# Performance work log

Hardware: AMD Instinct MI355X
Metric: run time of the kernel (lower is better)

The kernel has to match this reference:

```python
import jax, jax.numpy as jnp
import numpy as np

NUM_HEADS = 12


def setup_inputs() -> dict:
    key = jax.random.key(0)
    k1, k2, k3 = jax.random.split(key, 3)
    B, S, E = 1, 4096, 768
    x = jax.random.normal(k1, (B, S, E), dtype=jnp.float32)
    # learned parameters (nn.Linear weights, stored as [in, out] for x @ W)
    w_qkv = jax.random.normal(k2, (E, 3 * E), dtype=jnp.float32) * 0.02
    b_qkv = jnp.zeros((3 * E,), dtype=jnp.float32)
    w_out = jax.random.normal(k3, (E, E), dtype=jnp.float32) * 0.02
    b_out = jnp.zeros((E,), dtype=jnp.float32)
    return {"x": x, "w_qkv": w_qkv, "b_qkv": b_qkv, "w_out": w_out, "b_out": b_out}


def reference(x, w_qkv, b_qkv, w_out, b_out):
    """Single-process (world_size==1) path of the module:
    qkv projection -> multi-head scaled-dot-product softmax attention
    (non-causal) -> output projection. Dropout is identity in eval.
    """
    B, S, E = x.shape
    H = NUM_HEADS
    D = E // H
    scale = 1.0 / jnp.sqrt(jnp.asarray(D, dtype=x.dtype))

    qkv = x @ w_qkv + b_qkv                       # [B, S, 3E]
    qkv = qkv.reshape(B, S, 3, H, D)
    qkv = jnp.transpose(qkv, (2, 0, 3, 1, 4))     # [3, B, H, S, D]
    q, k, v = qkv[0], qkv[1], qkv[2]

    scores = jnp.einsum("bhqd,bhkd->bhqk", q * scale, k)  # [B, H, S, S]
    attn = jax.nn.softmax(scores, axis=-1)
    out = jnp.einsum("bhqk,bhkd->bhqd", attn, v)           # [B, H, S, D]

    out = jnp.transpose(out, (0, 2, 1, 3)).reshape(B, S, E)
    return out @ w_out + b_out
```

## Files before the change

### kernel.cpp

```cpp
#include <hip/hip_runtime.h>

typedef __attribute__((ext_vector_type(8))) short bh8;
typedef __attribute__((ext_vector_type(4))) float fx4;

__device__ __forceinline__ unsigned short f2bf(float f) {
    unsigned int u = __float_as_uint(f);
    u += 0x7FFF + ((u >> 16) & 1);
    return (unsigned short)(u >> 16);
}

__device__ __forceinline__ unsigned int cvtpk_bf16(float a, float b) {
    unsigned int r;
    asm("v_cvt_pk_bf16_f32 %0, %1, %2" : "=v"(r) : "v"(a), "v"(b));
    return r;
}

__device__ __forceinline__ bh8 pack4(unsigned int a, unsigned int b,
                                     unsigned int c, unsigned int d) {
    union { unsigned int u[4]; bh8 h; } z;
    z.u[0] = a; z.u[1] = b; z.u[2] = c; z.u[3] = d;
    return z.h;
}

__device__ __forceinline__ void stage_rows8(const unsigned short* g, long ldg,
                                            unsigned short* lds, int lane) {
    int r8 = lane >> 3;
    int gc = (lane & 7) ^ r8;
    __builtin_amdgcn_global_load_lds(
        (const __attribute__((address_space(1))) void*)(g + (long)r8 * ldg + gc * 8),
        (__attribute__((address_space(3))) void*)lds, 16, 0, 0);
}

__device__ __forceinline__ bh8 frag_ld(const unsigned short* t, int row, int kchunk, int lane) {
    int ch = (kchunk + (lane >> 4)) ^ (row & 7);
    return *(const bh8*)(t + row * 64 + ch * 8);
}

__global__ __launch_bounds__(256) void castbf(const float* __restrict__ x,
                                              unsigned short* __restrict__ y, int n) {
    int i = (blockIdx.x * 256 + threadIdx.x) * 4;
    if (i < n) {
        float4 v = *(const float4*)(x + i);
        ushort4 o = make_ushort4(f2bf(v.x), f2bf(v.y), f2bf(v.z), f2bf(v.w));
        *(ushort4*)(y + i) = o;
    }
}

__global__ __launch_bounds__(256) void transW(const float* __restrict__ W,
                                              unsigned short* __restrict__ Wt,
                                              int K, int N) {
    __shared__ float t[32][33];
    const int n0 = blockIdx.x * 32, k0 = blockIdx.y * 32;
    const int tx = threadIdx.x & 31, ty = threadIdx.x >> 5;
    #pragma unroll
    for (int r = ty; r < 32; r += 8)
        t[r][tx] = W[(size_t)(k0 + r) * N + n0 + tx];
    __syncthreads();
    #pragma unroll
    for (int r = ty; r < 32; r += 8)
        Wt[(size_t)(n0 + r) * K + k0 + tx] = f2bf(t[tx][r]);
}

__global__ __launch_bounds__(256) void transV(const unsigned short* __restrict__ qkv,
                                              unsigned short* __restrict__ vt) {
    __shared__ unsigned short t[64][65];
    const int s0 = blockIdx.x * 64, h = blockIdx.y;
    const int tx = threadIdx.x & 63, ty = threadIdx.x >> 6;
    #pragma unroll
    for (int r = ty; r < 64; r += 4)
        t[r][tx] = qkv[(size_t)(s0 + r) * 2304 + 1536 + h * 64 + tx];
    __syncthreads();
    const int px = (tx & 32) + ((tx & 16) >> 2) + ((tx & 12) << 1) + (tx & 3);
    #pragma unroll
    for (int r = ty; r < 64; r += 4)
        vt[((size_t)h * 64 + r) * 4096 + s0 + px] = t[tx][r];
}

__global__ __launch_bounds__(256) void gemm_qkv(const unsigned short* __restrict__ A,
                                                const unsigned short* __restrict__ Bt,
                                                const float* __restrict__ bias,
                                                unsigned short* __restrict__ Cout,
                                                int M, int N, int K) {
    __shared__ __align__(16) unsigned short Ash[64 * 64];
    __shared__ __align__(16) unsigned short Bsh[128 * 64];
    const int m0 = blockIdx.y * 64, n0 = blockIdx.x * 128;
    const int tid = threadIdx.x, wid = tid >> 6, lane = tid & 63;
    const int wr = (wid >> 1) * 32, wc = (wid & 1) * 64;

    fx4 acc[2][4];
    #pragma unroll
    for (int i = 0; i < 2; ++i)
        #pragma unroll
        for (int j = 0; j < 4; ++j)
            acc[i][j] = (fx4){0.f, 0.f, 0.f, 0.f};

    for (int k0 = 0; k0 < K; k0 += 64) {
        #pragma unroll
        for (int g = 0; g < 2; ++g) {
            int rt = (wid * 2 + g) * 8;
            stage_rows8(A + (size_t)(m0 + rt) * K + k0, K, Ash + rt * 64, lane);
        }
        #pragma unroll
        for (int g = 0; g < 4; ++g) {
            int rt = (wid * 4 + g) * 8;
            stage_rows8(Bt + (size_t)(n0 + rt) * K + k0, K, Bsh + rt * 64, lane);
        }
        __syncthreads();
        #pragma unroll
        for (int ks = 0; ks < 2; ++ks) {
            bh8 af[2], bfr[4];
            #pragma unroll
            for (int i = 0; i < 2; ++i) af[i] = frag_ld(Ash, wr + i * 16 + (lane & 15), ks * 4, lane);
            #pragma unroll
            for (int j = 0; j < 4; ++j) bfr[j] = frag_ld(Bsh, wc + j * 16 + (lane & 15), ks * 4, lane);
            #pragma unroll
            for (int i = 0; i < 2; ++i)
                #pragma unroll
                for (int j = 0; j < 4; ++j)
                    acc[i][j] = __builtin_amdgcn_mfma_f32_16x16x32_bf16(af[i], bfr[j], acc[i][j], 0, 0, 0);
        }
        __syncthreads();
    }

    const int cc = lane & 15, g4 = (lane >> 4) * 4;
    #pragma unroll
    for (int j = 0; j < 4; ++j) {
        int col = n0 + wc + j * 16 + cc;
        float bv = bias[col];
        float sc = (col < 768) ? 0.18033688011112042f : 1.0f;
        #pragma unroll
        for (int i = 0; i < 2; ++i) {
            #pragma unroll
            for (int r = 0; r < 4; ++r) {
                int row = m0 + wr + i * 16 + g4 + r;
                Cout[(size_t)row * N + col] = f2bf((acc[i][j][r] + bv) * sc);
            }
        }
    }
}

__global__ __launch_bounds__(256) void gemm64(const unsigned short* __restrict__ A,
                                              const unsigned short* __restrict__ Bt,
                                              const float* __restrict__ bias,
                                              float* __restrict__ Cout,
                                              int M, int N, int K) {
    __shared__ __align__(16) unsigned short Ash[64 * 64];
    __shared__ __align__(16) unsigned short Bsh[64 * 64];
    const int m0 = blockIdx.y * 64, n0 = blockIdx.x * 64;
    const int tid = threadIdx.x, wid = tid >> 6, lane = tid & 63;
    const int wr = (wid >> 1) * 32, wc = (wid & 1) * 32;

    fx4 acc[2][2];
    #pragma unroll
    for (int i = 0; i < 2; ++i)
        #pragma unroll
        for (int j = 0; j < 2; ++j)
            acc[i][j] = (fx4){0.f, 0.f, 0.f, 0.f};

    for (int k0 = 0; k0 < K; k0 += 64) {
        #pragma unroll
        for (int g = 0; g < 2; ++g) {
            int rt = (wid * 2 + g) * 8;
            stage_rows8(A + (size_t)(m0 + rt) * K + k0, K, Ash + rt * 64, lane);
            stage_rows8(Bt + (size_t)(n0 + rt) * K + k0, K, Bsh + rt * 64, lane);
        }
        __syncthreads();
        #pragma unroll
        for (int ks = 0; ks < 2; ++ks) {
            bh8 af[2], bfr[2];
            #pragma unroll
            for (int i = 0; i < 2; ++i) af[i] = frag_ld(Ash, wr + i * 16 + (lane & 15), ks * 4, lane);
            #pragma unroll
            for (int j = 0; j < 2; ++j) bfr[j] = frag_ld(Bsh, wc + j * 16 + (lane & 15), ks * 4, lane);
            #pragma unroll
            for (int i = 0; i < 2; ++i)
                #pragma unroll
                for (int j = 0; j < 2; ++j)
                    acc[i][j] = __builtin_amdgcn_mfma_f32_16x16x32_bf16(af[i], bfr[j], acc[i][j], 0, 0, 0);
        }
        __syncthreads();
    }

    const int cc = lane & 15, g4 = (lane >> 4) * 4;
    #pragma unroll
    for (int j = 0; j < 2; ++j) {
        int col = n0 + wc + j * 16 + cc;
        float bv = bias[col];
        #pragma unroll
        for (int i = 0; i < 2; ++i) {
            #pragma unroll
            for (int r = 0; r < 4; ++r) {
                int row = m0 + wr + i * 16 + g4 + r;
                Cout[(size_t)row * N + col] = acc[i][j][r] + bv;
            }
        }
    }
}

__global__ __launch_bounds__(256) void attn_fwd(const unsigned short* __restrict__ qkv,
                                                const unsigned short* __restrict__ vt,
                                                unsigned short* __restrict__ ao) {
    __shared__ __align__(16) char smem[40960];
    unsigned short* Qs  = (unsigned short*)smem;
    unsigned short* Ks0 = (unsigned short*)(smem + 8192);
    unsigned short* Ks1 = (unsigned short*)(smem + 16384);
    unsigned short* Vs0 = (unsigned short*)(smem + 24576);
    unsigned short* Vs1 = (unsigned short*)(smem + 32768);
    float* Of    = (float*)smem;
    float* l_lds = (float*)(smem + 17408);

    const int h = blockIdx.y, q0 = blockIdx.x * 64;
    const int tid = threadIdx.x, wid = tid >> 6, lane = tid & 63;
    const int g = lane >> 4, qc = lane & 15, x = qc & 7;
    const int wq = wid >> 1, wk = wid & 1;

    const unsigned short* qg_ = qkv + (size_t)q0 * 2304 + h * 64;
    const unsigned short* kgb = qkv + 768 + h * 64;
    const unsigned short* vgb = vt + (size_t)h * 64 * 4096;

    #pragma unroll
    for (int gg = 0; gg < 2; ++gg) {
        int rt = (wid * 2 + gg) * 8;
        stage_rows8(qg_ + (size_t)rt * 2304, 2304, Qs + rt * 64, lane);
        stage_rows8(kgb + (size_t)rt * 2304, 2304, Ks0 + rt * 64, lane);
        stage_rows8(vgb + (size_t)rt * 4096, 4096, Vs0 + rt * 64, lane);
    }
    __syncthreads();

    bh8 qf[2][2];
    #pragma unroll
    for (int qg = 0; qg < 2; ++qg)
        #pragma unroll
        for (int kc = 0; kc < 2; ++kc)
            qf[qg][kc] = frag_ld(Qs, 32 * wq + 16 * qg + qc, 4 * kc, lane);

    int koff[2][2], voff[4];
    #pragma unroll
    for (int jm = 0; jm < 2; ++jm)
        #pragma unroll
        for (int kc = 0; kc < 2; ++kc)
            koff[jm][kc] = (32 * wk + 16 * jm + qc) * 64 + ((4 * kc + g) ^ x) * 8;
    #pragma unroll
    for (int dj = 0; dj < 4; ++dj)
        voff[dj] = (16 * dj + qc) * 64 + ((4 * wk + g) ^ x) * 8;

    float lrun[2] = {0.f, 0.f};
    fx4 oacP[4][2];
    #pragma unroll
    for (int dj = 0; dj < 4; ++dj)
        #pragma unroll
        for (int qg = 0; qg < 2; ++qg)
            oacP[dj][qg] = (fx4){0.f, 0.f, 0.f, 0.f};

    const unsigned short* knext = kgb + (size_t)64 * 2304;
    const unsigned short* vnext = vgb + 64;

    auto tile_step = [&](const unsigned short* Kc, const unsigned short* Vc,
                         unsigned short* Kd, unsigned short* Vd, bool pref) {
        if (pref) {
            #pragma unroll
            for (int gg = 0; gg < 2; ++gg) {
                int rt = (wid * 2 + gg) * 8;
                stage_rows8(knext + (size_t)rt * 2304, 2304, Kd + rt * 64, lane);
                stage_rows8(vnext + (size_t)rt * 4096, 4096, Vd + rt * 64, lane);
            }
            knext += (size_t)64 * 2304;
            vnext += 64;
        }

        bh8 kf[2][2];
        #pragma unroll
        for (int jm = 0; jm < 2; ++jm) {
            kf[jm][0] = *(const bh8*)(Kc + koff[jm][0]);
            kf[jm][1] = *(const bh8*)(Kc + koff[jm][1]);
        }
        fx4 sT[2][2];
        __builtin_amdgcn_s_setprio(1);
        #pragma unroll
        for (int jm = 0; jm < 2; ++jm)
            #pragma unroll
            for (int qg = 0; qg < 2; ++qg) {
                fx4 z = (fx4){0.f, 0.f, 0.f, 0.f};
                z = __builtin_amdgcn_mfma_f32_16x16x32_bf16(kf[jm][0], qf[qg][0], z, 0, 0, 0);
                z = __builtin_amdgcn_mfma_f32_16x16x32_bf16(kf[jm][1], qf[qg][1], z, 0, 0, 0);
                sT[jm][qg] = z;
            }
        __builtin_amdgcn_s_setprio(0);

        #pragma unroll
        for (int jm = 0; jm < 2; ++jm)
            #pragma unroll
            for (int qg = 0; qg < 2; ++qg) {
                sT[jm][qg][0] = __builtin_amdgcn_exp2f(sT[jm][qg][0]);
                sT[jm][qg][1] = __builtin_amdgcn_exp2f(sT[jm][qg][1]);
                sT[jm][qg][2] = __builtin_amdgcn_exp2f(sT[jm][qg][2]);
                sT[jm][qg][3] = __builtin_amdgcn_exp2f(sT[jm][qg][3]);
                lrun[qg] += (sT[jm][qg][0] + sT[jm][qg][1]) + (sT[jm][qg][2] + sT[jm][qg][3]);
            }

        bh8 vf[4];
        #pragma unroll
        for (int dj = 0; dj < 4; ++dj) vf[dj] = *(const bh8*)(Vc + voff[dj]);
        __builtin_amdgcn_s_setprio(1);
        #pragma unroll
        for (int qg = 0; qg < 2; ++qg) {
            bh8 pb = pack4(cvtpk_bf16(sT[0][qg][0], sT[0][qg][1]),
                           cvtpk_bf16(sT[0][qg][2], sT[0][qg][3]),
                           cvtpk_bf16(sT[1][qg][0], sT[1][qg][1]),
                           cvtpk_bf16(sT[1][qg][2], sT[1][qg][3]));
            #pragma unroll
            for (int dj = 0; dj < 4; ++dj)
                oacP[dj][qg] = __builtin_amdgcn_mfma_f32_16x16x32_bf16(vf[dj], pb, oacP[dj][qg], 0, 0, 0);
        }
        __builtin_amdgcn_s_setprio(0);
        __syncthreads();
    };

    for (int t2 = 0; t2 < 32; ++t2) {
        tile_step(Ks0, Vs0, Ks1, Vs1, true);
        tile_step(Ks1, Vs1, Ks0, Vs0, t2 < 31);
    }

    #pragma unroll
    for (int qg = 0; qg < 2; ++qg) {
        lrun[qg] += __shfl_xor(lrun[qg], 16);
        lrun[qg] += __shfl_xor(lrun[qg], 32);
    }
    if (wk == 1) {
        #pragma unroll
        for (int qg = 0; qg < 2; ++qg) {
            int q = 32 * wq + 16 * qg + qc;
            #pragma unroll
            for (int dj = 0; dj < 4; ++dj)
                *(fx4*)(Of + q * 68 + 16 * dj + 4 * g) = oacP[dj][qg];
            l_lds[q] = lrun[qg];
        }
    }
    __syncthreads();
    if (wk == 0) {
        #pragma unroll
        for (int qg = 0; qg < 2; ++qg) {
            int q = 32 * wq + 16 * qg + qc;
            float inv = 1.0f / (lrun[qg] + l_lds[q]);
            unsigned short* aop = ao + (size_t)(q0 + q) * 768 + h * 64;
            #pragma unroll
            for (int dj = 0; dj < 4; ++dj) {
                fx4 o = oacP[dj][qg];
                fx4 p = *(const fx4*)(Of + q * 68 + 16 * dj + 4 * g);
                int d0 = dj * 16 + 4 * g;
                *(unsigned int*)(aop + d0)     = cvtpk_bf16((o[0] + p[0]) * inv, (o[1] + p[1]) * inv);
                *(unsigned int*)(aop + d0 + 2) = cvtpk_bf16((o[2] + p[2]) * inv, (o[3] + p[3]) * inv);
            }
        }
    }
}

extern "C" void kernel_launch(void* const* d_in, const int* in_sizes, int n_in,
                              void* d_out, int out_size, void* d_ws, size_t ws_size,
                              hipStream_t stream) {
    const float* x     = (const float*)d_in[0];
    const float* w_qkv = (const float*)d_in[1];
    const float* b_qkv = (const float*)d_in[2];
    const float* w_out = (const float*)d_in[3];
    const float* b_out = (const float*)d_in[4];
    float* out = (float*)d_out;

    const int S = 4096, E = 768, E3 = 2304, H = 12;

    unsigned short* xb    = (unsigned short*)d_ws;
    unsigned short* wqkvT = xb    + (size_t)S * E;
    unsigned short* woutT = wqkvT + (size_t)E3 * E;
    unsigned short* qkvb  = woutT + (size_t)E * E;
    unsigned short* vtp   = qkvb  + (size_t)S * E3;
    unsigned short* ao    = vtp   + (size_t)H * 64 * S;

    castbf<<<dim3((S * E) / (256 * 4)), 256, 0, stream>>>(x, xb, S * E);
    transW<<<dim3(E3 / 32, E / 32), 256, 0, stream>>>(w_qkv, wqkvT, E, E3);
    transW<<<dim3(E / 32, E / 32), 256, 0, stream>>>(w_out, woutT, E, E);
    gemm_qkv<<<dim3(E3 / 128, S / 64), 256, 0, stream>>>(xb, wqkvT, b_qkv, qkvb, S, E3, E);
    transV<<<dim3(S / 64, H), 256, 0, stream>>>(qkvb, vtp);
    attn_fwd<<<dim3(S / 64, H), 256, 0, stream>>>(qkvb, vtp, ao);
    gemm64<<<dim3(E / 64, S / 64), 256, 0, stream>>>(ao, woutT, b_out, out, S, E, E);
}
```

Baseline: 124.7 us.

## Fuse V transpose into QKV GEMM epilogue and double-buffer GEMM k-loops

The QKV GEMM now writes the V slice straight into the transposed, permuted layout through a shared-memory scratch in its epilogue, which removes the separate transV kernel launch and its extra global read and write of V. Both GEMMs also double-buffer their LDS tiles, prefetching the next k-slab before computing the current one, so global loads overlap with MFMA work. The cost is more LDS per block (48KB and 32KB), which can lower occupancy. Q and K blocks no longer write V columns to qkvb, so qkvb's V region is left unwritten.

After: 119.2 us. 1.05x faster.

```diff
diff --git a/kernel.cpp b/kernel.cpp
--- a/kernel.cpp
+++ b/kernel.cpp
@@ -61,32 +61,35 @@
         Wt[(size_t)(n0 + r) * K + k0 + tx] = f2bf(t[tx][r]);
 }
 
-__global__ __launch_bounds__(256) void transV(const unsigned short* __restrict__ qkv,
-                                              unsigned short* __restrict__ vt) {
-    __shared__ unsigned short t[64][65];
-    const int s0 = blockIdx.x * 64, h = blockIdx.y;
-    const int tx = threadIdx.x & 63, ty = threadIdx.x >> 6;
-    #pragma unroll
-    for (int r = ty; r < 64; r += 4)
-        t[r][tx] = qkv[(size_t)(s0 + r) * 2304 + 1536 + h * 64 + tx];
-    __syncthreads();
-    const int px = (tx & 32) + ((tx & 16) >> 2) + ((tx & 12) << 1) + (tx & 3);
-    #pragma unroll
-    for (int r = ty; r < 64; r += 4)
-        vt[((size_t)h * 64 + r) * 4096 + s0 + px] = t[tx][r];
-}
-
 __global__ __launch_bounds__(256) void gemm_qkv(const unsigned short* __restrict__ A,
                                                 const unsigned short* __restrict__ Bt,
                                                 const float* __restrict__ bias,
                                                 unsigned short* __restrict__ Cout,
-                                                int M, int N, int K) {
-    __shared__ __align__(16) unsigned short Ash[64 * 64];
-    __shared__ __align__(16) unsigned short Bsh[128 * 64];
+                                                unsigned short* __restrict__ vt) {
+    const int M = 4096, N = 2304, K = 768;
+    __shared__ __align__(16) char smem[49152];
+    unsigned short* Ash0 = (unsigned short*)smem;
+    unsigned short* Ash1 = (unsigned short*)(smem + 8192);
+    unsigned short* Bsh0 = (unsigned short*)(smem + 16384);
+    unsigned short* Bsh1 = (unsigned short*)(smem + 32768);
+    unsigned short* Tsc  = (unsigned short*)smem;
+
     const int m0 = blockIdx.y * 64, n0 = blockIdx.x * 128;
     const int tid = threadIdx.x, wid = tid >> 6, lane = tid & 63;
     const int wr = (wid >> 1) * 32, wc = (wid & 1) * 64;
 
+    #pragma unroll
+    for (int g = 0; g < 2; ++g) {
+        int rt = (wid * 2 + g) * 8;
+        stage_rows8(A + (size_t)(m0 + rt) * K, K, Ash0 + rt * 64, lane);
+    }
+    #pragma unroll
+    for (int g = 0; g < 4; ++g) {
+        int rt = (wid * 4 + g) * 8;
+        stage_rows8(Bt + (size_t)(n0 + rt) * K, K, Bsh0 + rt * 64, lane);
+    }
+    __syncthreads();
+
     fx4 acc[2][4];
     #pragma unroll
     for (int i = 0; i < 2; ++i)
@@ -94,25 +97,29 @@
         for (int j = 0; j < 4; ++j)
             acc[i][j] = (fx4){0.f, 0.f, 0.f, 0.f};
 
-    for (int k0 = 0; k0 < K; k0 += 64) {
-        #pragma unroll
-        for (int g = 0; g < 2; ++g) {
-            int rt = (wid * 2 + g) * 8;
-            stage_rows8(A + (size_t)(m0 + rt) * K + k0, K, Ash + rt * 64, lane);
-        }
-        #pragma unroll
-        for (int g = 0; g < 4; ++g) {
-            int rt = (wid * 4 + g) * 8;
-            stage_rows8(Bt + (size_t)(n0 + rt) * K + k0, K, Bsh + rt * 64, lane);
-        }
-        __syncthreads();
+    int kn = 64;
+    auto kstep = [&](const unsigned short* Ac, const unsigned short* Bc,
+                     unsigned short* Ad, unsigned short* Bd, bool pref) {
+        if (pref) {
+            #pragma unroll
+            for (int g = 0; g < 2; ++g) {
+                int rt = (wid * 2 + g) * 8;
+                stage_rows8(A + (size_t)(m0 + rt) * K + kn, K, Ad + rt * 64, lane);
+            }
+            #pragma unroll
+            for (int g = 0; g < 4; ++g) {
+                int rt = (wid * 4 + g) * 8;
+                stage_rows8(Bt + (size_t)(n0 + rt) * K + kn, K, Bd + rt * 64, lane);
+            }
+            kn += 64;
+        }
         #pragma unroll
         for (int ks = 0; ks < 2; ++ks) {
             bh8 af[2], bfr[4];
             #pragma unroll
-            for (int i = 0; i < 2; ++i) af[i] = frag_ld(Ash, wr + i * 16 + (lane & 15), ks * 4, lane);
-            #pragma unroll
-            for (int j = 0; j < 4; ++j) bfr[j] = frag_ld(Bsh, wc + j * 16 + (lane & 15), ks * 4, lane);
+            for (int i = 0; i < 2; ++i) af[i] = frag_ld(Ac, wr + i * 16 + (lane & 15), ks * 4, lane);
+            #pragma unroll
+            for (int j = 0; j < 4; ++j) bfr[j] = frag_ld(Bc, wc + j * 16 + (lane & 15), ks * 4, lane);
             #pragma unroll
             for (int i = 0; i < 2; ++i)
                 #pragma unroll
@@ -120,21 +127,53 @@
                     acc[i][j] = __builtin_amdgcn_mfma_f32_16x16x32_bf16(af[i], bfr[j], acc[i][j], 0, 0, 0);
         }
         __syncthreads();
+    };
+
+    for (int t2 = 0; t2 < 6; ++t2) {
+        kstep(Ash0, Bsh0, Ash1, Bsh1, true);
+        kstep(Ash1, Bsh1, Ash0, Bsh0, t2 < 5);
     }
 
     const int cc = lane & 15, g4 = (lane >> 4) * 4;
-    #pragma unroll
-    for (int j = 0; j < 4; ++j) {
-        int col = n0 + wc + j * 16 + cc;
-        float bv = bias[col];
-        float sc = (col < 768) ? 0.18033688011112042f : 1.0f;
-        #pragma unroll
-        for (int i = 0; i < 2; ++i) {
-            #pragma unroll
-            for (int r = 0; r < 4; ++r) {
-                int row = m0 + wr + i * 16 + g4 + r;
-                Cout[(size_t)row * N + col] = f2bf((acc[i][j][r] + bv) * sc);
-            }
+    if (n0 < 1536) {
+        #pragma unroll
+        for (int j = 0; j < 4; ++j) {
+            int col = n0 + wc + j * 16 + cc;
+            float bv = bias[col];
+            float sc = (col < 768) ? 0.18033688011112042f : 1.0f;
+            #pragma unroll
+            for (int i = 0; i < 2; ++i) {
+                #pragma unroll
+                for (int r = 0; r < 4; ++r) {
+                    int row = m0 + wr + i * 16 + g4 + r;
+                    Cout[(size_t)row * N + col] = f2bf((acc[i][j][r] + bv) * sc);
+                }
+            }
+        }
+    } else {
+        #pragma unroll
+        for (int j = 0; j < 4; ++j) {
+            int dloc = wc + j * 16 + cc;
+            float bv = bias[n0 + dloc];
+            #pragma unroll
+            for (int i = 0; i < 2; ++i) {
+                int sloc = wr + i * 16 + g4;
+                unsigned int u0 = cvtpk_bf16(acc[i][j][0] + bv, acc[i][j][1] + bv);
+                unsigned int u1 = cvtpk_bf16(acc[i][j][2] + bv, acc[i][j][3] + bv);
+                *(uint2*)(Tsc + dloc * 68 + sloc) = make_uint2(u0, u1);
+            }
+        }
+        __syncthreads();
+        const int d = tid >> 1, hf = (tid & 1) << 5;
+        const unsigned short* srow = Tsc + d * 68;
+        unsigned short* dst = vt + (size_t)(n0 - 1536 + d) * 4096 + m0 + hf;
+        #pragma unroll
+        for (int k = 0; k < 4; ++k) {
+            int y = hf + 8 * k;
+            int sb = (y & 32) + ((y & 24) >> 1);
+            uint2 lo = *(const uint2*)(srow + sb);
+            uint2 hi = *(const uint2*)(srow + sb + 16);
+            *(uint4*)(dst + 8 * k) = make_uint4(lo.x, lo.y, hi.x, hi.y);
         }
     }
 }
@@ -144,12 +183,20 @@
                                               const float* __restrict__ bias,
                                               float* __restrict__ Cout,
                                               int M, int N, int K) {
-    __shared__ __align__(16) unsigned short Ash[64 * 64];
-    __shared__ __align__(16) unsigned short Bsh[64 * 64];
+    __shared__ __align__(16) unsigned short Ash[2][64 * 64];
+    __shared__ __align__(16) unsigned short Bsh[2][64 * 64];
     const int m0 = blockIdx.y * 64, n0 = blockIdx.x * 64;
     const int tid = threadIdx.x, wid = tid >> 6, lane = tid & 63;
     const int wr = (wid >> 1) * 32, wc = (wid & 1) * 32;
 
+    #pragma unroll
+    for (int g = 0; g < 2; ++g) {
+        int rt = (wid * 2 + g) * 8;
+        stage_rows8(A + (size_t)(m0 + rt) * K, K, Ash[0] + rt * 64, lane);
+        stage_rows8(Bt + (size_t)(n0 + rt) * K, K, Bsh[0] + rt * 64, lane);
+    }
+    __syncthreads();
+
     fx4 acc[2][2];
     #pragma unroll
     for (int i = 0; i < 2; ++i)
@@ -157,21 +204,25 @@
         for (int j = 0; j < 2; ++j)
             acc[i][j] = (fx4){0.f, 0.f, 0.f, 0.f};
 
-    for (int k0 = 0; k0 < K; k0 += 64) {
-        #pragma unroll
-        for (int g = 0; g < 2; ++g) {
-            int rt = (wid * 2 + g) * 8;
-            stage_rows8(A + (size_t)(m0 + rt) * K + k0, K, Ash + rt * 64, lane);
-            stage_rows8(Bt + (size_t)(n0 + rt) * K + k0, K, Bsh + rt * 64, lane);
-        }
-        __syncthreads();
+    int kn = 64;
+    auto kstep = [&](const unsigned short* Ac, const unsigned short* Bc,
+                     unsigned short* Ad, unsigned short* Bd, bool pref) {
+        if (pref) {
+            #pragma unroll
+            for (int g = 0; g < 2; ++g) {
+                int rt = (wid * 2 + g) * 8;
+                stage_rows8(A + (size_t)(m0 + rt) * K + kn, K, Ad + rt * 64, lane);
+                stage_rows8(Bt + (size_t)(n0 + rt) * K + kn, K, Bd + rt * 64, lane);
+            }
+            kn += 64;
+        }
         #pragma unroll
         for (int ks = 0; ks < 2; ++ks) {
             bh8 af[2], bfr[2];
             #pragma unroll
-            for (int i = 0; i < 2; ++i) af[i] = frag_ld(Ash, wr + i * 16 + (lane & 15), ks * 4, lane);
-            #pragma unroll
-            for (int j = 0; j < 2; ++j) bfr[j] = frag_ld(Bsh, wc + j * 16 + (lane & 15), ks * 4, lane);
+            for (int i = 0; i < 2; ++i) af[i] = frag_ld(Ac, wr + i * 16 + (lane & 15), ks * 4, lane);
+            #pragma unroll
+            for (int j = 0; j < 2; ++j) bfr[j] = frag_ld(Bc, wc + j * 16 + (lane & 15), ks * 4, lane);
             #pragma unroll
             for (int i = 0; i < 2; ++i)
                 #pragma unroll
@@ -179,6 +230,11 @@
                     acc[i][j] = __builtin_amdgcn_mfma_f32_16x16x32_bf16(af[i], bfr[j], acc[i][j], 0, 0, 0);
         }
         __syncthreads();
+    };
+
+    for (int t2 = 0; t2 < 6; ++t2) {
+        kstep(Ash[0], Bsh[0], Ash[1], Bsh[1], true);
+        kstep(Ash[1], Bsh[1], Ash[0], Bsh[0], t2 < 5);
     }
 
     const int cc = lane & 15, g4 = (lane >> 4) * 4;
@@ -377,8 +433,7 @@
     castbf<<<dim3((S * E) / (256 * 4)), 256, 0, stream>>>(x, xb, S * E);
     transW<<<dim3(E3 / 32, E / 32), 256, 0, stream>>>(w_qkv, wqkvT, E, E3);
     transW<<<dim3(E / 32, E / 32), 256, 0, stream>>>(w_out, woutT, E, E);
-    gemm_qkv<<<dim3(E3 / 128, S / 64), 256, 0, stream>>>(xb, wqkvT, b_qkv, qkvb, S, E3, E);
-    transV<<<dim3(S / 64, H), 256, 0, stream>>>(qkvb, vtp);
+    gemm_qkv<<<dim3(E3 / 128, S / 64), 256, 0, stream>>>(xb, wqkvT, b_qkv, qkvb, vtp);
     attn_fwd<<<dim3(S / 64, H), 256, 0, stream>>>(qkvb, vtp, ao);
     gemm64<<<dim3(E / 64, S / 64), 256, 0, stream>>>(ao, woutT, b_out, out, S, E, E);
 }
```
